# Kernel optimization log

Measured on AMD Instinct MI355X. Metric: run time of the kernel, lower is better.

The kernel has to match this reference:

```python
import jax, jax.numpy as jnp
import numpy as np

MUL = 32            # multiplicity of 0e and 1o irreps
IN_DIM = MUL * 4    # 32 scalars + 32 vectors = 128
SH_DIM = 4          # 1x0e + 1x1o
N_EDGE_FEAT = 128
HIDDEN = 128
W_NUMEL = 4 * MUL * MUL  # 4 CG paths, uvw weights 32x1x32 each
EPS = 1e-5
INV_SQRT3 = 1.0 / np.sqrt(3.0)
PATH_NORM = 1.0 / np.sqrt(2.0 * MUL)  # 2 paths per output irrep, fan-in MUL


def _fc(edge_attr, W1, b1, W2, b2):
    h = jax.nn.relu(edge_attr @ W1 + b1)
    return h @ W2 + b2  # [E, W_NUMEL]


def _tensor_product(x, sh, w):
    # FullyConnectedTensorProduct for (32x0e+32x1o) x (1x0e+1x1o) -> (32x0e+32x1o)
    # CG (real w3j): 0x0->0: 1 ; 0x1->1, 1x0->1, 1x1->0: delta/sqrt(3)
    E = x.shape[0]
    x0 = x[:, :MUL]                      # [E,32]   scalars
    x1 = x[:, MUL:].reshape(E, MUL, 3)   # [E,32,3] vectors
    sh0 = sh[:, 0]                       # [E]
    sh1 = sh[:, 1:4]                     # [E,3]
    wA = w[:, 0 * MUL * MUL:1 * MUL * MUL].reshape(E, MUL, MUL)  # 0e x 0e -> 0e
    wB = w[:, 1 * MUL * MUL:2 * MUL * MUL].reshape(E, MUL, MUL)  # 0e x 1o -> 1o
    wC = w[:, 2 * MUL * MUL:3 * MUL * MUL].reshape(E, MUL, MUL)  # 1o x 0e -> 1o
    wD = w[:, 3 * MUL * MUL:4 * MUL * MUL].reshape(E, MUL, MUL)  # 1o x 1o -> 0e
    out0 = PATH_NORM * (
        jnp.einsum('eu,euw->ew', x0 * sh0[:, None], wA)
        + INV_SQRT3 * jnp.einsum('eui,ei,euw->ew', x1, sh1, wD))
    out1 = PATH_NORM * INV_SQRT3 * (
        jnp.einsum('eu,ei,euw->ewi', x0, sh1, wB)
        + jnp.einsum('eui,euw->ewi', x1 * sh0[:, None, None], wC))
    return jnp.concatenate([out0, out1.reshape(E, MUL * 3)], axis=-1)  # [E,128]


def _batch_norm(x, bn_weight, bn_bias):
    # e3nn-style equivariant BatchNorm (training stats): scalars get mean/var
    # normalization + affine; vectors get norm normalization + scale.
    N = x.shape[0]
    s = x[:, :MUL]                       # [N,32]
    v = x[:, MUL:].reshape(N, MUL, 3)    # [N,32,3]
    s = s - s.mean(axis=0)
    s = s * (jax.lax.rsqrt((s ** 2).mean(axis=0) + EPS) * bn_weight[:MUL]) + bn_bias
    v_norm = jax.lax.rsqrt((v ** 2).mean(axis=-1).mean(axis=0) + EPS)  # [32]
    v = v * (v_norm * bn_weight[MUL:])[None, :, None]
    return jnp.concatenate([s, v.reshape(N, MUL * 3)], axis=-1)


def _forward(node_attr, edge_index, edge_attr, edge_sh,
             W1, b1, W2, b2, bn_weight, bn_bias):
    edge_src, edge_dst = edge_index[0], edge_index[1]
    N = node_attr.shape[0]
    w = _fc(edge_attr, W1, b1, W2, b2)                     # [E, 4096]
    tp = _tensor_product(node_attr[edge_dst], edge_sh, w)  # [E, 128]
    # scatter mean over edge_src
    summed = jax.ops.segment_sum(tp, edge_src, num_segments=N)
    counts = jax.ops.segment_sum(jnp.ones((tp.shape[0],), tp.dtype), edge_src,
                                 num_segments=N)
    out = summed / jnp.maximum(counts, 1.0)[:, None]
    out = out + node_attr                                  # residual (same dim, pad=0)
    return _batch_norm(out, bn_weight, bn_bias)


def setup_inputs() -> dict:
    key = jax.random.key(0)
    ks = jax.random.split(key, 10)
    N, E = 10000, 60000
    node_attr = jax.random.normal(ks[0], (N, IN_DIM), jnp.float32)
    edge_index = jax.random.randint(ks[1], (2, E), 0, N)
    edge_attr = jax.random.normal(ks[2], (E, N_EDGE_FEAT), jnp.float32)
    edge_sh = jax.random.normal(ks[3], (E, SH_DIM), jnp.float32)
    W1 = jax.random.normal(ks[4], (N_EDGE_FEAT, HIDDEN), jnp.float32) / np.sqrt(N_EDGE_FEAT)
    b1 = jnp.zeros((HIDDEN,), jnp.float32)
    W2 = jax.random.normal(ks[5], (HIDDEN, W_NUMEL), jnp.float32) / np.sqrt(HIDDEN)
    b2 = jnp.zeros((W_NUMEL,), jnp.float32)
    bn_weight = jnp.ones((2 * MUL,), jnp.float32)
    bn_bias = jnp.zeros((MUL,), jnp.float32)
    return {"node_attr": node_attr, "edge_index": edge_index,
            "edge_attr": edge_attr, "edge_sh": edge_sh,
            "W1": W1, "b1": b1, "W2": W2, "b2": b2,
            "bn_weight": bn_weight, "bn_bias": bn_bias}


def reference(node_attr, edge_index, edge_attr, edge_sh,
              W1, b1, W2, b2, bn_weight, bn_bias):
    return _forward(node_attr, edge_index, edge_attr, edge_sh,
                    W1, b1, W2, b2, bn_weight, bn_bias)
```

## Files before the change

kernel.cpp:

```cpp
#include <hip/hip_runtime.h>
#include <math.h>

#define EPSV 1e-5f
#define IS3  0.57735026918962576f
#define PNRM 0.125f

typedef __attribute__((ext_vector_type(8)))  short  short8;
typedef __attribute__((ext_vector_type(16))) float  floatx16;

static __device__ inline unsigned short f2bf(float f) {
    unsigned int u = __float_as_uint(f);
    return (unsigned short)((u + 0x7fff + ((u >> 16) & 1)) >> 16);
}
static __device__ inline float bflo(unsigned int u) { return __uint_as_float(u << 16); }
static __device__ inline float bfhi(unsigned int u) { return __uint_as_float(u & 0xffff0000u); }

#define GLD16(gp, lp) __builtin_amdgcn_global_load_lds( \
    (const __attribute__((address_space(1))) unsigned int*)(gp), \
    (__attribute__((address_space(3))) unsigned int*)(lp), 16, 0, 0)

__global__ __launch_bounds__(256) void k0_tile(const float* __restrict__ W2,
                                               const float* __restrict__ W1,
                                               unsigned short* __restrict__ W2T,
                                               unsigned short* __restrict__ W1T) {
    const int bx = blockIdx.x, tid = threadIdx.x;
    __shared__ float tile[128 * 33];
    const float* src;
    unsigned short* dst;
    int nc, tb;
    if (bx < 128) { src = W2; dst = W2T; nc = 4096; tb = bx; }
    else          { src = W1; dst = W1T; nc = 128;  tb = bx - 128; }
    const int c0 = tb * 32;
#pragma unroll
    for (int r = 0; r < 16; ++r) {
        int lin = r * 256 + tid;
        int k = lin >> 5, c = lin & 31;
        tile[k * 33 + c] = src[(size_t)k * nc + c0 + c];
    }
    __syncthreads();
#pragma unroll
    for (int r = 0; r < 2; ++r) {
        int g = r * 256 + tid;
        int kc = g >> 5, c = g & 31;
        short8 v;
#pragma unroll
        for (int j = 0; j < 8; ++j)
            v[j] = (short)f2bf(tile[(kc * 8 + j) * 33 + c]);
        *(short8*)(dst + (size_t)tb * 4096 + kc * 256 + c * 8) = v;
    }
}

__global__ __launch_bounds__(256) void k1_fc(const float* __restrict__ ea,
                                             const unsigned short* __restrict__ W1T,
                                             const float* __restrict__ b1,
                                             const int* __restrict__ ei,
                                             unsigned short* __restrict__ hsw,
                                             int* __restrict__ deg, int E) {
    __shared__ __align__(16) unsigned short W1s[16384];
    __shared__ __align__(16) unsigned short bounce[4 * 1056];
    const int tid = threadIdx.x, lane = tid & 63, wv = tid >> 6;
    const int half = lane >> 5, col = lane & 31;
    const int e0 = blockIdx.x * 128;

    if (tid < 128) { int e = e0 + tid; if (e < E) atomicAdd(&deg[ei[e]], 1); }

#pragma unroll
    for (int q = 0; q < 8; ++q) {
        int chunk = wv * 8 + q;
        GLD16((const char*)W1T + chunk * 1024 + lane * 16, (char*)W1s + chunk * 1024);
    }

    int e = e0 + wv * 32 + col; if (e >= E) e = E - 1;
    short8 afr[8];
#pragma unroll
    for (int c = 0; c < 8; ++c) {
        const float4* p = (const float4*)(ea + (size_t)e * 128 + c * 16 + half * 8);
        float4 f0 = p[0], f1 = p[1];
        short8 v;
        v[0] = (short)f2bf(f0.x); v[1] = (short)f2bf(f0.y);
        v[2] = (short)f2bf(f0.z); v[3] = (short)f2bf(f0.w);
        v[4] = (short)f2bf(f1.x); v[5] = (short)f2bf(f1.y);
        v[6] = (short)f2bf(f1.z); v[7] = (short)f2bf(f1.w);
        afr[c] = v;
    }
    __syncthreads();

    unsigned short* myb = bounce + wv * 1056;
    const int gg = blockIdx.x * 4 + wv;
#pragma unroll
    for (int jt = 0; jt < 4; ++jt) {
        floatx16 d = {0,0,0,0,0,0,0,0,0,0,0,0,0,0,0,0};
#pragma unroll
        for (int c = 0; c < 8; ++c) {
            short8 bf = *(const short8*)((const char*)W1s + jt * 8192 + (2 * c + half) * 512 + col * 16);
            d = __builtin_amdgcn_mfma_f32_32x32x16_bf16(afr[c], bf, d, 0, 0, 0);
        }
        float b1v = b1[jt * 32 + col];
#pragma unroll
        for (int reg = 0; reg < 16; ++reg) {
            int r = (reg & 3) + 8 * (reg >> 2) + 4 * half;
            float v = d[reg] + b1v;
            v = v > 0.f ? v : 0.f;
            myb[(col >> 3) * 264 + r * 8 + (col & 7)] = f2bf(v);
        }
#pragma unroll
        for (int s = 0; s < 2; ++s) {
            short8 v = *(const short8*)&myb[(s * 2 + (lane >> 5)) * 264 + (lane & 31) * 8];
            *(short8*)(hsw + (size_t)gg * 4096 + jt * 1024 + s * 512 + lane * 8) = v;
        }
    }
}

__global__ __launch_bounds__(256, 2) void k2_mfma(const unsigned short* __restrict__ hsw,
                                                  const unsigned short* __restrict__ W2T,
                                                  const float* __restrict__ b2,
                                                  const float* __restrict__ na,
                                                  const int* __restrict__ ei,
                                                  const float* __restrict__ sh,
                                                  float* __restrict__ pre, int E) {
    __shared__ __align__(16) char smem[32768];
    unsigned short* Ctb = (unsigned short*)smem;
    float* red = (float*)smem;

    const int tid = threadIdx.x, lane = tid & 63, wv = tid >> 6;
    const int half = lane >> 5, col = lane & 31;
    const int ust = wv >> 1, esub = wv & 1;
    const int e0 = blockIdx.x * 64;

    for (int idx = tid; idx < 2048; idx += 256) {
        int el = idx & 63, u = idx >> 6;
        int e = e0 + el; int ec = e < E ? e : E - 1;
        int dn = ei[E + ec];
        const float* nar = na + (size_t)dn * 128;
        float x0  = nar[u];
        float x10 = nar[32 + u * 3], x11 = nar[33 + u * 3], x12 = nar[34 + u * 3];
        const float* shr = sh + (size_t)ec * 4;
        float s0 = shr[0], s1 = shr[1], s2 = shr[2], s3 = shr[3];
        int o = u * 64 + el;
        Ctb[0 * 2048 + o] = f2bf(PNRM * x0 * s0);
        Ctb[1 * 2048 + o] = f2bf(PNRM * IS3 * x0);
        Ctb[2 * 2048 + o] = f2bf(PNRM * IS3 * s0 * x10);
        Ctb[3 * 2048 + o] = f2bf(PNRM * IS3 * s0 * x11);
        Ctb[4 * 2048 + o] = f2bf(PNRM * IS3 * s0 * x12);
        Ctb[5 * 2048 + o] = f2bf(PNRM * IS3 * (x10 * s1 + x11 * s2 + x12 * s3));
    }

    const int gg = blockIdx.x * 2 + esub;
    short8 afr[8];
#pragma unroll
    for (int c = 0; c < 8; ++c)
        afr[c] = *(const short8*)(hsw + (size_t)gg * 4096 + (2 * c + half) * 256 + col * 8);

    __syncthreads();

    float acc0[16] = {}, accB[16] = {}, accC0[16] = {}, accC1[16] = {}, accC2[16] = {};
    const int elb0 = esub * 32 + half * 4;
    const unsigned short* bbase = W2T + half * 256 + col * 8;

#define LOADB(p, br, b2r) do {                                         \
        int _ct = 2 * (p) + ust;                                       \
        const unsigned short* _bp = bbase + (size_t)_ct * 4096;        \
        _Pragma("unroll")                                              \
        for (int _c = 0; _c < 8; ++_c)                                 \
            (br)[_c] = *(const short8*)(_bp + _c * 512);               \
        (b2r) = b2[_ct * 32 + col];                                    \
    } while (0)

#define COMPUTE(p, br, b2v) do {                                                              \
        const int _ct = 2 * (p) + ust;                                                        \
        const int _b = _ct >> 5, _u = _ct & 31;                                               \
        floatx16 d = {0,0,0,0,0,0,0,0,0,0,0,0,0,0,0,0};                                       \
        _Pragma("unroll")                                                                     \
        for (int _c = 0; _c < 8; ++_c)                                                        \
            d = __builtin_amdgcn_mfma_f32_32x32x16_bf16(afr[_c], (br)[_c], d, 0, 0, 0);       \
        if (_b == 0 || _b == 3) {                                                             \
            const unsigned short* tb = Ctb + (_b == 0 ? 0 : 5) * 2048;                        \
            _Pragma("unroll")                                                                 \
            for (int q = 0; q < 4; ++q) {                                                     \
                uint2 cv = *(const uint2*)&tb[_u * 64 + elb0 + q * 8];                        \
                acc0[q * 4 + 0] += bflo(cv.x) * (d[q * 4 + 0] + (b2v));                       \
                acc0[q * 4 + 1] += bfhi(cv.x) * (d[q * 4 + 1] + (b2v));                       \
                acc0[q * 4 + 2] += bflo(cv.y) * (d[q * 4 + 2] + (b2v));                       \
                acc0[q * 4 + 3] += bfhi(cv.y) * (d[q * 4 + 3] + (b2v));                       \
            }                                                                                 \
        } else if (_b == 1) {                                                                 \
            _Pragma("unroll")                                                                 \
            for (int q = 0; q < 4; ++q) {                                                     \
                uint2 cv = *(const uint2*)&Ctb[1 * 2048 + _u * 64 + elb0 + q * 8];            \
                accB[q * 4 + 0] += bflo(cv.x) * (d[q * 4 + 0] + (b2v));                       \
                accB[q * 4 + 1] += bfhi(cv.x) * (d[q * 4 + 1] + (b2v));                       \
                accB[q * 4 + 2] += bflo(cv.y) * (d[q * 4 + 2] + (b2v));                       \
                accB[q * 4 + 3] += bfhi(cv.y) * (d[q * 4 + 3] + (b2v));                       \
            }                                                                                 \
        } else {                                                                              \
            _Pragma("unroll")                                                                 \
            for (int q = 0; q < 4; ++q) {                                                     \
                uint2 cu0 = *(const uint2*)&Ctb[2 * 2048 + _u * 64 + elb0 + q * 8];           \
                uint2 cu1 = *(const uint2*)&Ctb[3 * 2048 + _u * 64 + elb0 + q * 8];           \
                uint2 cu2 = *(const uint2*)&Ctb[4 * 2048 + _u * 64 + elb0 + q * 8];           \
                float f0[4] = {bflo(cu0.x), bfhi(cu0.x), bflo(cu0.y), bfhi(cu0.y)};           \
                float f1[4] = {bflo(cu1.x), bfhi(cu1.x), bflo(cu1.y), bfhi(cu1.y)};           \
                float f2[4] = {bflo(cu2.x), bfhi(cu2.x), bflo(cu2.y), bfhi(cu2.y)};           \
                _Pragma("unroll")                                                             \
                for (int rr = 0; rr < 4; ++rr) {                                              \
                    float v = d[q * 4 + rr] + (b2v);                                          \
                    accC0[q * 4 + rr] += f0[rr] * v;                                          \
                    accC1[q * 4 + rr] += f1[rr] * v;                                          \
                    accC2[q * 4 + rr] += f2[rr] * v;                                          \
                }                                                                             \
            }                                                                                 \
        }                                                                                     \
    } while (0)

    short8 bA[8], bB[8], bC[8];
    float b2A, b2B, b2C;
    LOADB(0, bA, b2A); LOADB(1, bB, b2B); LOADB(2, bC, b2C);
    for (int p = 0; p < 60; p += 3) {
        COMPUTE(p,     bA, b2A); LOADB(p + 3, bA, b2A);
        COMPUTE(p + 1, bB, b2B); LOADB(p + 4, bB, b2B);
        COMPUTE(p + 2, bC, b2C); LOADB(p + 5, bC, b2C);
    }
    COMPUTE(60, bA, b2A); LOADB(63, bA, b2A);
    COMPUTE(61, bB, b2B);
    COMPUTE(62, bC, b2C);
    COMPUTE(63, bA, b2A);
#undef LOADB
#undef COMPUTE

    __syncthreads();
    if (ust == 1) {
#pragma unroll
        for (int q = 0; q < 4; ++q) {
#pragma unroll
            for (int rr = 0; rr < 4; ++rr) {
                int reg = q * 4 + rr;
                int el = esub * 32 + q * 8 + half * 4 + rr;
                int e = e0 + el; int ec = e < E ? e : E - 1;
                float4 sv = *(const float4*)(sh + (size_t)ec * 4);
                red[(((esub * 4 + 0) * 16 + reg) << 6) + lane] = acc0[reg];
                red[(((esub * 4 + 1) * 16 + reg) << 6) + lane] = sv.y * accB[reg] + accC0[reg];
                red[(((esub * 4 + 2) * 16 + reg) << 6) + lane] = sv.z * accB[reg] + accC1[reg];
                red[(((esub * 4 + 3) * 16 + reg) << 6) + lane] = sv.w * accB[reg] + accC2[reg];
            }
        }
    }
    __syncthreads();
    if (ust == 0) {
#pragma unroll
        for (int q = 0; q < 4; ++q) {
#pragma unroll
            for (int rr = 0; rr < 4; ++rr) {
                int reg = q * 4 + rr;
                int el = esub * 32 + q * 8 + half * 4 + rr;
                int e = e0 + el;
                if (e >= E) continue;
                float4 sv = *(const float4*)(sh + (size_t)e * 4);
                float a0 = acc0[reg] + red[(((esub * 4 + 0) * 16 + reg) << 6) + lane];
                float o0 = sv.y * accB[reg] + accC0[reg] + red[(((esub * 4 + 1) * 16 + reg) << 6) + lane];
                float o1 = sv.z * accB[reg] + accC1[reg] + red[(((esub * 4 + 2) * 16 + reg) << 6) + lane];
                float o2 = sv.w * accB[reg] + accC2[reg] + red[(((esub * 4 + 3) * 16 + reg) << 6) + lane];
                int s = ei[e];
                float* pr = pre + (size_t)s * 128;
                unsafeAtomicAdd(&pr[col], a0);
                unsafeAtomicAdd(&pr[32 + col * 3 + 0], o0);
                unsafeAtomicAdd(&pr[32 + col * 3 + 1], o1);
                unsafeAtomicAdd(&pr[32 + col * 3 + 2], o2);
            }
        }
    }
}

__global__ __launch_bounds__(256) void k4_finish(float* __restrict__ pre,
                                                 const int* __restrict__ deg,
                                                 const float* __restrict__ na,
                                                 float* __restrict__ stats, int N) {
    __shared__ float bns[96];
    const int tid = threadIdx.x;
    if (tid < 96) bns[tid] = 0.f;
    __syncthreads();
    const size_t total = (size_t)N * 128;
    for (size_t idx = (size_t)blockIdx.x * 256 + tid; idx < total;
         idx += (size_t)gridDim.x * 256) {
        int o = (int)(idx & 127);
        int n = (int)(idx >> 7);
        int dg = deg[n];
        float cf = (float)(dg > 0 ? dg : 1);
        float v = pre[idx] / cf + na[idx];
        pre[idx] = v;
        if (o < 32) {
            atomicAdd(&bns[o], v);
            atomicAdd(&bns[32 + o], v * v);
        } else {
            atomicAdd(&bns[64 + (o - 32) / 3], v * v);
        }
    }
    __syncthreads();
    if (tid < 96) atomicAdd(&stats[tid], bns[tid]);
}

__global__ __launch_bounds__(256) void k5_bn(const float* __restrict__ pre,
                                             const float* __restrict__ stats,
                                             const float* __restrict__ bnw,
                                             const float* __restrict__ bnb,
                                             float* __restrict__ out, int N) {
    size_t idx = (size_t)blockIdx.x * 256 + threadIdx.x;
    if (idx >= (size_t)N * 128) return;
    int o = (int)(idx & 127);
    float v = pre[idx];
    float invN = 1.f / (float)N;
    if (o < 32) {
        float m   = stats[o] * invN;
        float var = stats[32 + o] * invN - m * m;
        out[idx] = (v - m) * rsqrtf(var + EPSV) * bnw[o] + bnb[o];
    } else {
        int j = (o - 32) / 3;
        float vn = rsqrtf(stats[64 + j] * invN * (1.f / 3.f) + EPSV);
        out[idx] = v * vn * bnw[32 + j];
    }
}

extern "C" void kernel_launch(void* const* d_in, const int* in_sizes, int n_in,
                              void* d_out, int out_size, void* d_ws, size_t ws_size,
                              hipStream_t stream) {
    const float* node_attr  = (const float*)d_in[0];
    const int*   edge_index = (const int*)d_in[1];
    const float* edge_attr  = (const float*)d_in[2];
    const float* edge_sh    = (const float*)d_in[3];
    const float* W1  = (const float*)d_in[4];
    const float* b1  = (const float*)d_in[5];
    const float* W2  = (const float*)d_in[6];
    const float* b2  = (const float*)d_in[7];
    const float* bnw = (const float*)d_in[8];
    const float* bnb = (const float*)d_in[9];

    const int N = in_sizes[0] / 128;
    const int E = in_sizes[1] / 2;
    const int ngroups = ((E + 127) / 128) * 4;

    float* pre   = (float*)d_ws;
    float* stats = pre + (size_t)N * 128;
    int*   deg   = (int*)(stats + 96);
    char* pbase = (char*)(deg + N);
    pbase += (16 - ((size_t)pbase & 15)) & 15;
    unsigned short* hsw = (unsigned short*)pbase;
    unsigned short* W2T = hsw + (size_t)ngroups * 4096;
    unsigned short* W1T = W2T + (size_t)524288;

    hipMemsetAsync(pre, 0, ((size_t)N * 128 + 96 + (size_t)N) * sizeof(float), stream);

    k0_tile<<<132, 256, 0, stream>>>(W2, W1, W2T, W1T);
    k1_fc<<<(E + 127) / 128, 256, 0, stream>>>(edge_attr, W1T, b1, edge_index, hsw, deg, E);
    k2_mfma<<<(E + 63) / 64, 256, 0, stream>>>(hsw, W2T, b2, node_attr, edge_index,
                                               edge_sh, pre, E);
    k4_finish<<<1024, 256, 0, stream>>>(pre, deg, node_attr, stats, N);
    size_t ntot = (size_t)N * 128;
    k5_bn<<<(int)((ntot + 255) / 256), 256, 0, stream>>>(pre, stats, bnw, bnb,
                                                         (float*)d_out, N);
}
```

Before: 273.2 us.

## Replace atomic scatter-add with per-node edge slot lists and gather reduction

The MFMA kernel now writes each edge's tensor-product output to a per-edge buffer instead of issuing float atomics into the per-node accumulator. The FC kernel records each edge's index into a fixed-capacity slot list per source node. A new gather kernel sums the edges for each node, then normalises and accumulates the batch-norm statistics. This removes contention from the atomics and the large memset, but adds a write and re-read of about 30 MB of per-edge data. It also silently drops edges beyond 64 per node, which is only correct if degrees stay below that cap.

```diff
diff --git a/kernel.cpp b/kernel.cpp
--- a/kernel.cpp
+++ b/kernel.cpp
@@ -4,6 +4,7 @@
 #define EPSV 1e-5f
 #define IS3  0.57735026918962576f
 #define PNRM 0.125f
+#define SCAP 64
 
 typedef __attribute__((ext_vector_type(8)))  short  short8;
 typedef __attribute__((ext_vector_type(16))) float  floatx16;
@@ -55,14 +56,22 @@
                                              const float* __restrict__ b1,
                                              const int* __restrict__ ei,
                                              unsigned short* __restrict__ hsw,
-                                             int* __restrict__ deg, int E) {
+                                             int* __restrict__ deg,
+                                             int* __restrict__ slots, int E) {
     __shared__ __align__(16) unsigned short W1s[16384];
     __shared__ __align__(16) unsigned short bounce[4 * 1056];
     const int tid = threadIdx.x, lane = tid & 63, wv = tid >> 6;
     const int half = lane >> 5, col = lane & 31;
     const int e0 = blockIdx.x * 128;
 
-    if (tid < 128) { int e = e0 + tid; if (e < E) atomicAdd(&deg[ei[e]], 1); }
+    if (tid < 128) {
+        int e = e0 + tid;
+        if (e < E) {
+            int s = ei[e];
+            int pos = atomicAdd(&deg[s], 1);
+            if (pos < SCAP) slots[s * SCAP + pos] = e;
+        }
+    }
 
 #pragma unroll
     for (int q = 0; q < 8; ++q) {
@@ -117,7 +126,7 @@
                                                   const float* __restrict__ na,
                                                   const int* __restrict__ ei,
                                                   const float* __restrict__ sh,
-                                                  float* __restrict__ pre, int E) {
+                                                  float* __restrict__ tp, int E) {
     __shared__ __align__(16) char smem[32768];
     unsigned short* Ctb = (unsigned short*)smem;
     float* red = (float*)smem;
@@ -259,34 +268,46 @@
                 float o0 = sv.y * accB[reg] + accC0[reg] + red[(((esub * 4 + 1) * 16 + reg) << 6) + lane];
                 float o1 = sv.z * accB[reg] + accC1[reg] + red[(((esub * 4 + 2) * 16 + reg) << 6) + lane];
                 float o2 = sv.w * accB[reg] + accC2[reg] + red[(((esub * 4 + 3) * 16 + reg) << 6) + lane];
-                int s = ei[e];
-                float* pr = pre + (size_t)s * 128;
-                unsafeAtomicAdd(&pr[col], a0);
-                unsafeAtomicAdd(&pr[32 + col * 3 + 0], o0);
-                unsafeAtomicAdd(&pr[32 + col * 3 + 1], o1);
-                unsafeAtomicAdd(&pr[32 + col * 3 + 2], o2);
+                float* tpe = tp + (size_t)e * 128;
+                tpe[col] = a0;
+                tpe[32 + col * 3 + 0] = o0;
+                tpe[32 + col * 3 + 1] = o1;
+                tpe[32 + col * 3 + 2] = o2;
             }
         }
     }
 }
 
-__global__ __launch_bounds__(256) void k4_finish(float* __restrict__ pre,
+__global__ __launch_bounds__(256) void k4_gather(const float* __restrict__ tp,
                                                  const int* __restrict__ deg,
+                                                 const int* __restrict__ slots,
                                                  const float* __restrict__ na,
+                                                 float* __restrict__ pre,
                                                  float* __restrict__ stats, int N) {
     __shared__ float bns[96];
     const int tid = threadIdx.x;
     if (tid < 96) bns[tid] = 0.f;
     __syncthreads();
-    const size_t total = (size_t)N * 128;
-    for (size_t idx = (size_t)blockIdx.x * 256 + tid; idx < total;
-         idx += (size_t)gridDim.x * 256) {
-        int o = (int)(idx & 127);
-        int n = (int)(idx >> 7);
+    const int o = tid & 127, hf = tid >> 7;
+    for (int n = blockIdx.x * 2 + hf; n < N; n += gridDim.x * 2) {
         int dg = deg[n];
+        int cnt = dg < SCAP ? dg : SCAP;
+        const int* sl = slots + (size_t)n * SCAP;
+        float s = 0.f;
+        int j = 0;
+        for (; j + 4 <= cnt; j += 4) {
+            int4 e4 = *(const int4*)(sl + j);
+            float t0 = tp[(size_t)e4.x * 128 + o];
+            float t1 = tp[(size_t)e4.y * 128 + o];
+            float t2 = tp[(size_t)e4.z * 128 + o];
+            float t3 = tp[(size_t)e4.w * 128 + o];
+            s += (t0 + t1) + (t2 + t3);
+        }
+        for (; j < cnt; ++j)
+            s += tp[(size_t)sl[j] * 128 + o];
         float cf = (float)(dg > 0 ? dg : 1);
-        float v = pre[idx] / cf + na[idx];
-        pre[idx] = v;
+        float v = s / cf + na[(size_t)n * 128 + o];
+        pre[(size_t)n * 128 + o] = v;
         if (o < 32) {
             atomicAdd(&bns[o], v);
             atomicAdd(&bns[32 + o], v * v);
@@ -337,22 +358,25 @@
     const int E = in_sizes[1] / 2;
     const int ngroups = ((E + 127) / 128) * 4;
 
-    float* pre   = (float*)d_ws;
+    float* tp    = (float*)d_ws;
+    float* pre   = tp + (size_t)E * 128;
     float* stats = pre + (size_t)N * 128;
     int*   deg   = (int*)(stats + 96);
-    char* pbase = (char*)(deg + N);
+    int*   slots = deg + N;
+    char* pbase = (char*)(slots + (size_t)N * SCAP);
     pbase += (16 - ((size_t)pbase & 15)) & 15;
     unsigned short* hsw = (unsigned short*)pbase;
     unsigned short* W2T = hsw + (size_t)ngroups * 4096;
     unsigned short* W1T = W2T + (size_t)524288;
 
-    hipMemsetAsync(pre, 0, ((size_t)N * 128 + 96 + (size_t)N) * sizeof(float), stream);
+    hipMemsetAsync(stats, 0, (96 + (size_t)N) * sizeof(int), stream);
 
     k0_tile<<<132, 256, 0, stream>>>(W2, W1, W2T, W1T);
-    k1_fc<<<(E + 127) / 128, 256, 0, stream>>>(edge_attr, W1T, b1, edge_index, hsw, deg, E);
+    k1_fc<<<(E + 127) / 128, 256, 0, stream>>>(edge_attr, W1T, b1, edge_index,
+                                               hsw, deg, slots, E);
     k2_mfma<<<(E + 63) / 64, 256, 0, stream>>>(hsw, W2T, b2, node_attr, edge_index,
-                                               edge_sh, pre, E);
-    k4_finish<<<1024, 256, 0, stream>>>(pre, deg, node_attr, stats, N);
+                                               edge_sh, tp, E);
+    k4_gather<<<2500, 256, 0, stream>>>(tp, deg, slots, node_attr, pre, stats, N);
     size_t ntot = (size_t)N * 128;
     k5_bn<<<(int)((ntot + 255) / 256), 256, 0, stream>>>(pre, stats, bnw, bnb,
                                                          (float*)d_out, N);
```

Result: no change. 277.4 us (+1.5%).
